# Optimization experiments

Measured on AMD Instinct MI355X. Metric: run time of the kernel, lower is better.

## Reference

```python
import jax, jax.numpy as jnp
import numpy as np

N_HEADS = 16  # emb_dim 512 // head_dim 32


def _heads(t, h=N_HEADS):
    b, n, d = t.shape
    return t.reshape(b, n, h, d // h).transpose(0, 2, 1, 3)  # [b h n hd]


def _merge(t):
    b, h, n, hd = t.shape
    return t.transpose(0, 2, 1, 3).reshape(b, n, h * hd)


def setup_inputs() -> dict:
    key = jax.random.key(0)
    ks = jax.random.split(key, 6)
    b, n, nc, d = 2, 2048, 256, 512
    x = jax.random.normal(ks[0], (b, n, d), dtype=jnp.float32)
    clusters = jax.random.normal(ks[1], (b, nc, d), dtype=jnp.float32)
    token_sizes = jax.random.uniform(ks[2], (b, n), dtype=jnp.float32)
    Wq = jax.random.normal(ks[3], (d, d), dtype=jnp.float32) * 0.02
    Wkv = jax.random.normal(ks[4], (d, 2 * d), dtype=jnp.float32) * 0.02
    Wo = jax.random.normal(ks[5], (d, d), dtype=jnp.float32) * 0.02
    return {"x": x, "clusters": clusters, "token_sizes": token_sizes,
            "Wq": Wq, "Wkv": Wkv, "Wo": Wo}


def reference(x, clusters, token_sizes, Wq, Wkv, Wo):
    b, n, d = x.shape
    hd = d // N_HEADS
    scale = hd ** -0.5

    q_in = jnp.concatenate([x, clusters], axis=1)       # pack tokens + clusters as queries
    q = _heads(q_in @ Wq)                               # [b h n+nc hd]
    kv = x @ Wkv                                        # [b n 2d]
    k = _heads(kv[..., :d])                             # [b h n hd]
    v = _heads(kv[..., d:])                             # [b h n hd]

    attn = jnp.einsum('bhqd,bhkd->bhqk', q, k) * scale  # [b h n+nc n]
    attn_x = attn[:, :, :n, :]                          # token queries  [b h n n]
    attn_c = attn[:, :, n:, :]                          # cluster queries [b h nc n]

    # soft assignment: softmax over cluster axis, then row-normalize
    a_c = jax.nn.softmax(attn_c, axis=-2)
    a_c = a_c / (jnp.sum(a_c, axis=-1, keepdims=True) + 1e-5)
    clusters_out = _merge(jnp.einsum('bhck,bhkd->bhcd', a_c, v)) @ Wo  # [b nc d]

    # additive log token-size bias on the query axis (as in the original)
    attn_x = attn_x + jnp.log(token_sizes + 1e-10)[:, None, :, None]
    a_x = jax.nn.softmax(attn_x, axis=-1)
    x_out = _merge(jnp.einsum('bhqk,bhkd->bhqd', a_x, v)) @ Wo  # [b n d]

    return x_out, clusters_out
```

## Files before the change

kernel.cpp:

```cpp
#include <hip/hip_runtime.h>
#include <hip/hip_bf16.h>

#define N_TOK 2048
#define N_CLU 256
#define N_ALL 2304
#define DMODEL 512
#define NH 16
#define HD 32
#define BATCH 2
#define EXPSCALE 0.25503486f

typedef short bf16x8 __attribute__((ext_vector_type(8)));
typedef float f32x4  __attribute__((ext_vector_type(4)));
typedef unsigned short u16;

static __device__ __forceinline__ u16 f2b(float x) {
    __hip_bfloat16 h = __float2bfloat16(x);
    return *reinterpret_cast<u16*>(&h);
}
static __device__ __forceinline__ unsigned int cvt_pk_bf16(float lo, float hi) {
    unsigned int r;
    asm("v_cvt_pk_bf16_f32 %0, %1, %2" : "=v"(r) : "v"(lo), "v"(hi));
    return r;
}
#if __has_builtin(__builtin_amdgcn_exp2f)
#define EXP2(x) __builtin_amdgcn_exp2f(x)
#else
#define EXP2(x) exp2f(x)
#endif
static __device__ __forceinline__ void async16(u16* lds, const u16* g) {
    __builtin_amdgcn_global_load_lds(
        (const __attribute__((address_space(1))) unsigned int*)g,
        (__attribute__((address_space(3))) unsigned int*)lds, 16, 0, 0);
}

__global__ __launch_bounds__(256) void cvt_bf16_k(const float* __restrict__ in,
                                                  u16* __restrict__ out)
{
    const long i = ((long)blockIdx.x * 256 + threadIdx.x) * 8;
    float4 a = *(const float4*)(in + i);
    float4 b = *(const float4*)(in + i + 4);
    u16 v[8] = { f2b(a.x), f2b(a.y), f2b(a.z), f2b(a.w),
                 f2b(b.x), f2b(b.y), f2b(b.z), f2b(b.w) };
    *(bf16x8*)(out + i) = *(const bf16x8*)v;
}

__global__ __launch_bounds__(256) void cvtT_k(const float* __restrict__ W,
                                              u16* __restrict__ WT,
                                              int R, int C, float scale)
{
    __shared__ float tile[32][33];
    const int tx = threadIdx.x & 31, ty = threadIdx.x >> 5;
    const int c0 = blockIdx.x * 32, r0 = blockIdx.y * 32;
    #pragma unroll
    for (int i = 0; i < 4; i++)
        tile[ty + i * 8][tx] = W[(long)(r0 + ty + i * 8) * C + c0 + tx];
    __syncthreads();
    #pragma unroll
    for (int i = 0; i < 4; i++)
        WT[(long)(c0 + ty + i * 8) * R + r0 + tx] = f2b(tile[tx][ty + i * 8] * scale);
}

__global__ __launch_bounds__(256) void gemm_bf16(
    const u16* __restrict__ A, long sA,
    const u16* __restrict__ BT,
    void* __restrict__ Cv, long sC,
    int N, int K, int mode)
{
    const int t = threadIdx.x;
    const int m0 = blockIdx.y * 128, n0 = blockIdx.x * 128;
    A += (long)blockIdx.z * sA;
    __shared__ u16 As[128 * 32];
    __shared__ u16 Bs[128 * 32];
    const int wid = t >> 6, lane = t & 63;
    const int lr = lane & 15, lg = lane >> 4;
    const int wr = wid >> 1, wc = wid & 1;
    f32x4 acc[4][4] = {};
    const int o1 = t * 16, o2 = o1 + 4096;
    const int row1 = o1 >> 6, ke1 = (o1 & 63) >> 1;
    const int row2 = o2 >> 6, ke2 = (o2 & 63) >> 1;
    for (int k0 = 0; k0 < K; k0 += 32) {
        async16(As + (o1 >> 1), A  + (long)(m0 + row1) * K + k0 + ke1);
        async16(As + (o2 >> 1), A  + (long)(m0 + row2) * K + k0 + ke2);
        async16(Bs + (o1 >> 1), BT + (long)(n0 + row1) * K + k0 + ke1);
        async16(Bs + (o2 >> 1), BT + (long)(n0 + row2) * K + k0 + ke2);
        __syncthreads();
        bf16x8 af[4], bfr[4];
        #pragma unroll
        for (int i = 0; i < 4; i++) {
            af[i]  = *(const bf16x8*)&As[(wr * 64 + i * 16 + lr) * 32 + lg * 8];
            bfr[i] = *(const bf16x8*)&Bs[(wc * 64 + i * 16 + lr) * 32 + lg * 8];
        }
        #pragma unroll
        for (int mi = 0; mi < 4; mi++)
            #pragma unroll
            for (int ni = 0; ni < 4; ni++)
                acc[mi][ni] = __builtin_amdgcn_mfma_f32_16x16x32_bf16(af[mi], bfr[ni], acc[mi][ni], 0, 0, 0);
        __syncthreads();
    }
    if (mode == 1) {
        float* C = (float*)Cv;
        #pragma unroll
        for (int mi = 0; mi < 4; mi++)
            #pragma unroll
            for (int ni = 0; ni < 4; ni++) {
                const int rbase = m0 + wr * 64 + mi * 16 + lg * 4;
                #pragma unroll
                for (int r = 0; r < 4; r++) {
                    int rw = rbase + r;
                    int bb = rw >= N_ALL;
                    int w  = rw - bb * N_ALL;
                    long orow = (w < N_TOK) ? ((long)bb * N_TOK + w)
                                            : (2L * N_TOK + (long)bb * N_CLU + (w - N_TOK));
                    C[orow * N + n0 + wc * 64 + ni * 16 + lr] = acc[mi][ni][r];
                }
            }
    } else {
        u16* C = (u16*)Cv + (long)blockIdx.z * sC;
        #pragma unroll
        for (int mi = 0; mi < 4; mi++)
            #pragma unroll
            for (int ni = 0; ni < 4; ni++) {
                const long rbase = m0 + wr * 64 + mi * 16 + lg * 4;
                #pragma unroll
                for (int r = 0; r < 4; r++)
                    C[(rbase + r) * N + n0 + wc * 64 + ni * 16 + lr] = f2b(acc[mi][ni][r]);
            }
    }
}

__global__ __launch_bounds__(256) void vt_prep(
    const u16* __restrict__ qkv, u16* __restrict__ vt)
{
    const int b = blockIdx.z, h = blockIdx.y, k0 = blockIdx.x * 64;
    const int t = threadIdx.x;
    __shared__ u16 tile[64][48];
    {
        const int key = t >> 2, dc = (t & 3) * 8;
        *(bf16x8*)&tile[key][dc] = *(const bf16x8*)(
            qkv + ((long)b * N_TOK + k0 + key) * 1536 + 1024 + h * HD + dc);
    }
    __syncthreads();
    {
        const int d = t & 31, kc = (t >> 5) * 8;
        bf16x8 v;
        #pragma unroll
        for (int i = 0; i < 8; i++) v[i] = (short)tile[kc + i][d];
        *(bf16x8*)(vt + (((long)(b * NH + h)) * HD + d) * N_TOK + k0 + kc) = v;
    }
}

__global__ __launch_bounds__(512) void attn_x3(
    const u16* __restrict__ qkv, const u16* __restrict__ vt,
    u16* __restrict__ aob)
{
    const int b = blockIdx.z, h = blockIdx.y;
    const int wid = threadIdx.x >> 6, lane = threadIdx.x & 63;
    const int lr = lane & 15, lg = lane >> 4;
    const int q0 = blockIdx.x * 128 + (wid & 3) * 32;
    const int khalf = wid >> 2;

    __shared__ unsigned int P[8][32][32];
    __shared__ float comb[4][64][18];
    __shared__ u16 Ot[4][32][40];

    unsigned int (*Pw)[32] = P[wid];
    const int sw = 4 * (lr & 7);

    bf16x8 qf[2];
    #pragma unroll
    for (int qs = 0; qs < 2; qs++)
        qf[qs] = *(const bf16x8*)(
            qkv + ((long)b * N_TOK + q0 + qs * 16 + lr) * 1536 + h * HD + lg * 8);

    f32x4 o[2][2] = {};
    float rs[2] = {0.f, 0.f};
    const u16* kbase = qkv + (long)b * N_TOK * 1536 + 512 + h * HD + lg * 8;
    const u16* vbase = vt + ((long)(b * NH + h)) * HD * N_TOK;

    const int kend = khalf * 1024 + 1024;
    for (int k0 = khalf * 1024; k0 < kend; k0 += 64) {
        bf16x8 kf[4];
        #pragma unroll
        for (int kg = 0; kg < 4; kg++)
            kf[kg] = *(const bf16x8*)(kbase + (long)(k0 + kg * 16 + lr) * 1536);
        #pragma unroll
        for (int qs = 0; qs < 2; qs++) {
            #pragma unroll
            for (int kg = 0; kg < 4; kg++) {
                f32x4 z = {0.f, 0.f, 0.f, 0.f};
                f32x4 s = __builtin_amdgcn_mfma_f32_16x16x32_bf16(kf[kg], qf[qs], z, 0, 0, 0);
                float e0 = EXP2(s[0]), e1 = EXP2(s[1]);
                float e2 = EXP2(s[2]), e3 = EXP2(s[3]);
                rs[qs] += (e0 + e1) + (e2 + e3);
                uint2 w = { cvt_pk_bf16(e0, e1), cvt_pk_bf16(e2, e3) };
                *(uint2*)&Pw[qs * 16 + lr][(kg * 8 + lg * 2) ^ sw] = w;
            }
        }
        #pragma unroll
        for (int c = 0; c < 2; c++) {
            bf16x8 pb0 = *(const bf16x8*)&Pw[lr][(c * 16 + lg * 4) ^ sw];
            bf16x8 pb1 = *(const bf16x8*)&Pw[16 + lr][(c * 16 + lg * 4) ^ sw];
            #pragma unroll
            for (int dg = 0; dg < 2; dg++) {
                bf16x8 vf = *(const bf16x8*)(
                    vbase + (long)(dg * 16 + lr) * N_TOK + k0 + c * 32 + lg * 8);
                o[0][dg] = __builtin_amdgcn_mfma_f32_16x16x32_bf16(vf, pb0, o[0][dg], 0, 0, 0);
                o[1][dg] = __builtin_amdgcn_mfma_f32_16x16x32_bf16(vf, pb1, o[1][dg], 0, 0, 0);
            }
        }
    }
    #pragma unroll
    for (int qs = 0; qs < 2; qs++) {
        rs[qs] += __shfl_xor(rs[qs], 16);
        rs[qs] += __shfl_xor(rs[qs], 32);
    }
    if (wid >= 4) {
        float* cp = &comb[wid - 4][lane][0];
        #pragma unroll
        for (int qs = 0; qs < 2; qs++)
            #pragma unroll
            for (int dg = 0; dg < 2; dg++)
                #pragma unroll
                for (int r = 0; r < 4; r++)
                    cp[qs * 8 + dg * 4 + r] = o[qs][dg][r];
        cp[16] = rs[0];
        cp[17] = rs[1];
    }
    __syncthreads();
    if (wid < 4) {
        const float* cp = &comb[wid][lane][0];
        #pragma unroll
        for (int qs = 0; qs < 2; qs++)
            #pragma unroll
            for (int dg = 0; dg < 2; dg++)
                #pragma unroll
                for (int r = 0; r < 4; r++)
                    o[qs][dg][r] += cp[qs * 8 + dg * 4 + r];
        rs[0] += cp[16];
        rs[1] += cp[17];
        const float inv0 = 1.f / rs[0], inv1 = 1.f / rs[1];
        #pragma unroll
        for (int dg = 0; dg < 2; dg++)
            #pragma unroll
            for (int r = 0; r < 4; r++) {
                Ot[wid][lr][dg * 16 + lg * 4 + r]      = f2b(o[0][dg][r] * inv0);
                Ot[wid][16 + lr][dg * 16 + lg * 4 + r] = f2b(o[1][dg][r] * inv1);
            }
        const int rrow = lane >> 2, seg = lane & 3;
        #pragma unroll
        for (int rep = 0; rep < 2; rep++) {
            bf16x8 v = *(const bf16x8*)&Ot[wid][rep * 16 + rrow][seg * 8];
            *(bf16x8*)(aob + ((long)b * N_ALL + q0 + rep * 16 + rrow) * DMODEL + h * HD + seg * 8) = v;
        }
    }
}

__global__ __launch_bounds__(256) void attn_c_mfma(
    const u16* __restrict__ qc, const u16* __restrict__ qkv,
    const u16* __restrict__ vt, float* __restrict__ part)
{
    const int b = blockIdx.z, h = blockIdx.y, kblk = blockIdx.x;
    const int wid = threadIdx.x >> 6, lane = threadIdx.x & 63;
    const int lr = lane & 15, lg = lane >> 4;
    const int c0 = wid * 64;

    __shared__ u16 Pl[4][64][72];
    __shared__ float cs2[64][4];
    u16 (*P)[72] = Pl[wid];

    bf16x8 qf[4];
    #pragma unroll
    for (int qs = 0; qs < 4; qs++)
        qf[qs] = *(const bf16x8*)(
            qc + ((long)(b * N_CLU) + c0 + qs * 16 + lr) * DMODEL + h * HD + lg * 8);

    f32x4 o[4][2] = {};
    float rs[4][4] = {};
    const u16* kbase = qkv + (long)b * N_TOK * 1536 + 512 + h * HD + lg * 8;
    const u16* vbase = vt + ((long)(b * NH + h)) * HD * N_TOK;

    for (int kt = 0; kt < 4; kt++) {
        const int k0 = kblk * 256 + kt * 64;
        bf16x8 kf[4];
        #pragma unroll
        for (int kg = 0; kg < 4; kg++)
            kf[kg] = *(const bf16x8*)(kbase + (long)(k0 + kg * 16 + lr) * 1536);
        f32x4 e[4][4];
        #pragma unroll
        for (int qs = 0; qs < 4; qs++)
            #pragma unroll
            for (int kg = 0; kg < 4; kg++) {
                f32x4 z = {0.f, 0.f, 0.f, 0.f};
                e[qs][kg] = __builtin_amdgcn_mfma_f32_16x16x32_bf16(qf[qs], kf[kg], z, 0, 0, 0);
            }
        float csum[4];
        #pragma unroll
        for (int kg = 0; kg < 4; kg++) {
            float v = 0.f;
            #pragma unroll
            for (int qs = 0; qs < 4; qs++)
                #pragma unroll
                for (int r = 0; r < 4; r++) {
                    float p = EXP2(e[qs][kg][r]);
                    e[qs][kg][r] = p;
                    v += p;
                }
            v += __shfl_xor(v, 16);
            v += __shfl_xor(v, 32);
            csum[kg] = v;
        }
        float own = (lg == 0) ? csum[0] : (lg == 1) ? csum[1] : (lg == 2) ? csum[2] : csum[3];
        __syncthreads();
        cs2[lane][wid] = own;
        __syncthreads();
        float ics0, ics1, ics2, ics3;
        {
            f32x4 c4;
            c4 = *(const f32x4*)&cs2[ 0 + lr][0]; ics0 = 1.f / (c4[0] + c4[1] + c4[2] + c4[3]);
            c4 = *(const f32x4*)&cs2[16 + lr][0]; ics1 = 1.f / (c4[0] + c4[1] + c4[2] + c4[3]);
            c4 = *(const f32x4*)&cs2[32 + lr][0]; ics2 = 1.f / (c4[0] + c4[1] + c4[2] + c4[3]);
            c4 = *(const f32x4*)&cs2[48 + lr][0]; ics3 = 1.f / (c4[0] + c4[1] + c4[2] + c4[3]);
        }
        #pragma unroll
        for (int qs = 0; qs < 4; qs++)
            #pragma unroll
            for (int kg = 0; kg < 4; kg++) {
                const float ics = (kg == 0) ? ics0 : (kg == 1) ? ics1 : (kg == 2) ? ics2 : ics3;
                #pragma unroll
                for (int r = 0; r < 4; r++) {
                    float p = e[qs][kg][r] * ics;
                    rs[qs][r] += p;
                    P[qs * 16 + lg * 4 + r][kg * 16 + lr] = f2b(p);
                }
            }
        #pragma unroll
        for (int kh = 0; kh < 2; kh++) {
            bf16x8 pf[4];
            #pragma unroll
            for (int qs = 0; qs < 4; qs++)
                pf[qs] = *(const bf16x8*)&P[qs * 16 + lr][kh * 32 + lg * 8];
            #pragma unroll
            for (int dg = 0; dg < 2; dg++) {
                bf16x8 vf = *(const bf16x8*)(
                    vbase + (long)(dg * 16 + lr) * N_TOK + k0 + kh * 32 + lg * 8);
                #pragma unroll
                for (int qs = 0; qs < 4; qs++)
                    o[qs][dg] = __builtin_amdgcn_mfma_f32_16x16x32_bf16(pf[qs], vf, o[qs][dg], 0, 0, 0);
            }
        }
    }
    float* pp = part + ((((long)(b * NH + h)) * 8 + kblk) * 256) * 36;
    #pragma unroll
    for (int qs = 0; qs < 4; qs++)
        #pragma unroll
        for (int r = 0; r < 4; r++) {
            const int row = c0 + qs * 16 + lg * 4 + r;
            pp[(long)row * 36 + lr]      = o[qs][0][r];
            pp[(long)row * 36 + 16 + lr] = o[qs][1][r];
            float v = rs[qs][r];
            v += __shfl_xor(v, 1); v += __shfl_xor(v, 2);
            v += __shfl_xor(v, 4); v += __shfl_xor(v, 8);
            if (lr == 0) pp[(long)row * 36 + 32] = v;
        }
}

__global__ __launch_bounds__(256) void attn_c_reduce(
    const float* __restrict__ part, u16* __restrict__ aob)
{
    const int gid = blockIdx.x * 256 + threadIdx.x;
    const int b = gid >> 12, h = (gid >> 8) & 15, c = gid & 255;
    float acc[32] = {};
    float rsum = 0.f;
    for (int j = 0; j < 8; j++) {
        const float* pp = part + ((((long)(b * NH + h)) * 8 + j) * 256 + c) * 36;
        #pragma unroll
        for (int e4 = 0; e4 < 8; e4++) {
            f32x4 v = *(const f32x4*)(pp + e4 * 4);
            acc[e4 * 4 + 0] += v[0]; acc[e4 * 4 + 1] += v[1];
            acc[e4 * 4 + 2] += v[2]; acc[e4 * 4 + 3] += v[3];
        }
        rsum += pp[32];
    }
    const float inv = 1.f / (rsum + 1e-5f);
    u16* orow = aob + ((long)b * N_ALL + N_TOK + c) * DMODEL + h * HD;
    #pragma unroll
    for (int e = 0; e < 32; e++) orow[e] = f2b(acc[e] * inv);
}

extern "C" void kernel_launch(void* const* d_in, const int* in_sizes, int n_in,
                              void* d_out, int out_size, void* d_ws, size_t ws_size,
                              hipStream_t stream)
{
    const float* x        = (const float*)d_in[0];
    const float* clusters = (const float*)d_in[1];
    const float* Wq  = (const float*)d_in[3];
    const float* Wkv = (const float*)d_in[4];
    const float* Wo  = (const float*)d_in[5];
    float* out = (float*)d_out;

    char* ws = (char*)d_ws;
    u16*   xb    = (u16*)(ws);
    u16*   cb    = (u16*)(ws + 4194304);
    u16*   WcatT = (u16*)(ws + 4718592);
    u16*   WoT   = (u16*)(ws + 6291456);
    u16*   qkv   = (u16*)(ws + 6815744);
    u16*   qc    = (u16*)(ws + 19398656);
    u16*   vt    = (u16*)(ws + 19922944);
    u16*   aob   = (u16*)(ws + 24117248);
    float* part  = (float*)(ws + 28835840);

    cvt_bf16_k<<<dim3(1024), 256, 0, stream>>>(x, xb);
    cvt_bf16_k<<<dim3(128),  256, 0, stream>>>(clusters, cb);
    cvtT_k<<<dim3(16, 16), 256, 0, stream>>>(Wq,  WcatT,             512,  512, EXPSCALE);
    cvtT_k<<<dim3(32, 16), 256, 0, stream>>>(Wkv, WcatT + 512 * 512, 512, 1024, 1.f);
    cvtT_k<<<dim3(16, 16), 256, 0, stream>>>(Wo,  WoT,               512,  512, 1.f);

    gemm_bf16<<<dim3(12, 16, 2), 256, 0, stream>>>(
        xb, (long)N_TOK * DMODEL, WcatT, qkv, (long)N_TOK * 1536, 1536, DMODEL, 0);
    gemm_bf16<<<dim3(4, 2, 2), 256, 0, stream>>>(
        cb, (long)N_CLU * DMODEL, WcatT, qc, (long)N_CLU * DMODEL, DMODEL, DMODEL, 0);

    vt_prep<<<dim3(32, 16, 2), 256, 0, stream>>>(qkv, vt);

    attn_x3<<<dim3(16, 16, 2), 512, 0, stream>>>(qkv, vt, aob);
    attn_c_mfma<<<dim3(8, 16, 2), 256, 0, stream>>>(qc, qkv, vt, part);
    attn_c_reduce<<<dim3(32), 256, 0, stream>>>(part, aob);

    gemm_bf16<<<dim3(4, 36, 1), 256, 0, stream>>>(
        aob, 0, WoT, out, 0, DMODEL, DMODEL, 1);
}
```

Baseline: 221.5 us.

## Split token attention key range four ways and widen cluster attention blocks

The token-query attention kernel now gives each block 64 queries and splits the key range across four waves per query group instead of two. That doubles the grid to raise occupancy and shorten each wave's serial loop. Partial outputs and row sums are combined through a shared-memory buffer that is reused from the P scratch space, which needs an extra barrier. The cluster attention kernel moves to 512 threads with 32 clusters per wave, which halves per-wave register state and widens the cross-wave column-sum reduction to eight entries.

```diff
diff --git a/kernel.cpp b/kernel.cpp
--- a/kernel.cpp
+++ b/kernel.cpp
@@ -150,51 +150,51 @@
     }
 }
 
-__global__ __launch_bounds__(512) void attn_x3(
+__global__ __launch_bounds__(512) void attn_x4(
     const u16* __restrict__ qkv, const u16* __restrict__ vt,
     u16* __restrict__ aob)
 {
     const int b = blockIdx.z, h = blockIdx.y;
     const int wid = threadIdx.x >> 6, lane = threadIdx.x & 63;
     const int lr = lane & 15, lg = lane >> 4;
-    const int q0 = blockIdx.x * 128 + (wid & 3) * 32;
-    const int khalf = wid >> 2;
-
-    __shared__ unsigned int P[8][32][32];
-    __shared__ float comb[4][64][18];
-    __shared__ u16 Ot[4][32][40];
-
-    unsigned int (*Pw)[32] = P[wid];
+    const int qs = wid & 1, kq = wid >> 1;
+    const int q0 = blockIdx.x * 64 + qs * 32;
+
+    __shared__ __align__(16) char smem[32768];
+    unsigned int (*Pw)[32] = (unsigned int (*)[32])(smem + wid * 4096);
+    float* combB = (float*)smem;
+    u16*   OtB   = (u16*)(smem + 27648);
+
     const int sw = 4 * (lr & 7);
 
     bf16x8 qf[2];
     #pragma unroll
-    for (int qs = 0; qs < 2; qs++)
-        qf[qs] = *(const bf16x8*)(
-            qkv + ((long)b * N_TOK + q0 + qs * 16 + lr) * 1536 + h * HD + lg * 8);
+    for (int qq = 0; qq < 2; qq++)
+        qf[qq] = *(const bf16x8*)(
+            qkv + ((long)b * N_TOK + q0 + qq * 16 + lr) * 1536 + h * HD + lg * 8);
 
     f32x4 o[2][2] = {};
     float rs[2] = {0.f, 0.f};
     const u16* kbase = qkv + (long)b * N_TOK * 1536 + 512 + h * HD + lg * 8;
     const u16* vbase = vt + ((long)(b * NH + h)) * HD * N_TOK;
 
-    const int kend = khalf * 1024 + 1024;
-    for (int k0 = khalf * 1024; k0 < kend; k0 += 64) {
+    const int kstart = kq * 512;
+    for (int k0 = kstart; k0 < kstart + 512; k0 += 64) {
         bf16x8 kf[4];
         #pragma unroll
         for (int kg = 0; kg < 4; kg++)
             kf[kg] = *(const bf16x8*)(kbase + (long)(k0 + kg * 16 + lr) * 1536);
         #pragma unroll
-        for (int qs = 0; qs < 2; qs++) {
+        for (int qq = 0; qq < 2; qq++) {
             #pragma unroll
             for (int kg = 0; kg < 4; kg++) {
                 f32x4 z = {0.f, 0.f, 0.f, 0.f};
-                f32x4 s = __builtin_amdgcn_mfma_f32_16x16x32_bf16(kf[kg], qf[qs], z, 0, 0, 0);
+                f32x4 s = __builtin_amdgcn_mfma_f32_16x16x32_bf16(kf[kg], qf[qq], z, 0, 0, 0);
                 float e0 = EXP2(s[0]), e1 = EXP2(s[1]);
                 float e2 = EXP2(s[2]), e3 = EXP2(s[3]);
-                rs[qs] += (e0 + e1) + (e2 + e3);
+                rs[qq] += (e0 + e1) + (e2 + e3);
                 uint2 w = { cvt_pk_bf16(e0, e1), cvt_pk_bf16(e2, e3) };
-                *(uint2*)&Pw[qs * 16 + lr][(kg * 8 + lg * 2) ^ sw] = w;
+                *(uint2*)&Pw[qq * 16 + lr][(kg * 8 + lg * 2) ^ sw] = w;
             }
         }
         #pragma unroll
@@ -211,72 +211,77 @@
         }
     }
     #pragma unroll
-    for (int qs = 0; qs < 2; qs++) {
-        rs[qs] += __shfl_xor(rs[qs], 16);
-        rs[qs] += __shfl_xor(rs[qs], 32);
-    }
-    if (wid >= 4) {
-        float* cp = &comb[wid - 4][lane][0];
-        #pragma unroll
-        for (int qs = 0; qs < 2; qs++)
+    for (int qq = 0; qq < 2; qq++) {
+        rs[qq] += __shfl_xor(rs[qq], 16);
+        rs[qq] += __shfl_xor(rs[qq], 32);
+    }
+    __syncthreads();
+    if (kq > 0) {
+        float* cp = combB + (((qs * 3 + kq - 1) * 64) + lane) * 18;
+        #pragma unroll
+        for (int qq = 0; qq < 2; qq++)
             #pragma unroll
             for (int dg = 0; dg < 2; dg++)
                 #pragma unroll
                 for (int r = 0; r < 4; r++)
-                    cp[qs * 8 + dg * 4 + r] = o[qs][dg][r];
+                    cp[qq * 8 + dg * 4 + r] = o[qq][dg][r];
         cp[16] = rs[0];
         cp[17] = rs[1];
     }
     __syncthreads();
-    if (wid < 4) {
-        const float* cp = &comb[wid][lane][0];
-        #pragma unroll
-        for (int qs = 0; qs < 2; qs++)
-            #pragma unroll
-            for (int dg = 0; dg < 2; dg++)
-                #pragma unroll
-                for (int r = 0; r < 4; r++)
-                    o[qs][dg][r] += cp[qs * 8 + dg * 4 + r];
-        rs[0] += cp[16];
-        rs[1] += cp[17];
+    if (kq == 0) {
+        #pragma unroll
+        for (int j = 0; j < 3; j++) {
+            const float* cp = combB + (((qs * 3 + j) * 64) + lane) * 18;
+            #pragma unroll
+            for (int qq = 0; qq < 2; qq++)
+                #pragma unroll
+                for (int dg = 0; dg < 2; dg++)
+                    #pragma unroll
+                    for (int r = 0; r < 4; r++)
+                        o[qq][dg][r] += cp[qq * 8 + dg * 4 + r];
+            rs[0] += cp[16];
+            rs[1] += cp[17];
+        }
         const float inv0 = 1.f / rs[0], inv1 = 1.f / rs[1];
+        u16* Ot = OtB + qs * 32 * 40;
         #pragma unroll
         for (int dg = 0; dg < 2; dg++)
             #pragma unroll
             for (int r = 0; r < 4; r++) {
-                Ot[wid][lr][dg * 16 + lg * 4 + r]      = f2b(o[0][dg][r] * inv0);
-                Ot[wid][16 + lr][dg * 16 + lg * 4 + r] = f2b(o[1][dg][r] * inv1);
+                Ot[lr * 40 + dg * 16 + lg * 4 + r]        = f2b(o[0][dg][r] * inv0);
+                Ot[(16 + lr) * 40 + dg * 16 + lg * 4 + r] = f2b(o[1][dg][r] * inv1);
             }
         const int rrow = lane >> 2, seg = lane & 3;
         #pragma unroll
         for (int rep = 0; rep < 2; rep++) {
-            bf16x8 v = *(const bf16x8*)&Ot[wid][rep * 16 + rrow][seg * 8];
+            bf16x8 v = *(const bf16x8*)&Ot[(rep * 16 + rrow) * 40 + seg * 8];
             *(bf16x8*)(aob + ((long)b * N_ALL + q0 + rep * 16 + rrow) * DMODEL + h * HD + seg * 8) = v;
         }
     }
 }
 
-__global__ __launch_bounds__(256) void attn_c_mfma(
+__global__ __launch_bounds__(512) void attn_c_mfma(
     const u16* __restrict__ qc, const u16* __restrict__ qkv,
     const u16* __restrict__ vt, float* __restrict__ part)
 {
     const int b = blockIdx.z, h = blockIdx.y, kblk = blockIdx.x;
     const int wid = threadIdx.x >> 6, lane = threadIdx.x & 63;
     const int lr = lane & 15, lg = lane >> 4;
-    const int c0 = wid * 64;
-
-    __shared__ u16 Pl[4][64][72];
-    __shared__ float cs2[64][4];
+    const int c0 = wid * 32;
+
+    __shared__ u16 Pl[8][32][72];
+    __shared__ float cs2[64][8];
     u16 (*P)[72] = Pl[wid];
 
-    bf16x8 qf[4];
-    #pragma unroll
-    for (int qs = 0; qs < 4; qs++)
+    bf16x8 qf[2];
+    #pragma unroll
+    for (int qs = 0; qs < 2; qs++)
         qf[qs] = *(const bf16x8*)(
             qc + ((long)(b * N_CLU) + c0 + qs * 16 + lr) * DMODEL + h * HD + lg * 8);
 
-    f32x4 o[4][2] = {};
-    float rs[4][4] = {};
+    f32x4 o[2][2] = {};
+    float rs[2][4] = {};
     const u16* kbase = qkv + (long)b * N_TOK * 1536 + 512 + h * HD + lg * 8;
     const u16* vbase = vt + ((long)(b * NH + h)) * HD * N_TOK;
 
@@ -286,9 +291,9 @@
         #pragma unroll
         for (int kg = 0; kg < 4; kg++)
             kf[kg] = *(const bf16x8*)(kbase + (long)(k0 + kg * 16 + lr) * 1536);
-        f32x4 e[4][4];
-        #pragma unroll
-        for (int qs = 0; qs < 4; qs++)
+        f32x4 e[2][4];
+        #pragma unroll
+        for (int qs = 0; qs < 2; qs++)
             #pragma unroll
             for (int kg = 0; kg < 4; kg++) {
                 f32x4 z = {0.f, 0.f, 0.f, 0.f};
@@ -299,7 +304,7 @@
         for (int kg = 0; kg < 4; kg++) {
             float v = 0.f;
             #pragma unroll
-            for (int qs = 0; qs < 4; qs++)
+            for (int qs = 0; qs < 2; qs++)
                 #pragma unroll
                 for (int r = 0; r < 4; r++) {
                     float p = EXP2(e[qs][kg][r]);
@@ -314,45 +319,43 @@
         __syncthreads();
         cs2[lane][wid] = own;
         __syncthreads();
-        float ics0, ics1, ics2, ics3;
-        {
-            f32x4 c4;
-            c4 = *(const f32x4*)&cs2[ 0 + lr][0]; ics0 = 1.f / (c4[0] + c4[1] + c4[2] + c4[3]);
-            c4 = *(const f32x4*)&cs2[16 + lr][0]; ics1 = 1.f / (c4[0] + c4[1] + c4[2] + c4[3]);
-            c4 = *(const f32x4*)&cs2[32 + lr][0]; ics2 = 1.f / (c4[0] + c4[1] + c4[2] + c4[3]);
-            c4 = *(const f32x4*)&cs2[48 + lr][0]; ics3 = 1.f / (c4[0] + c4[1] + c4[2] + c4[3]);
-        }
-        #pragma unroll
-        for (int qs = 0; qs < 4; qs++)
+        float ics[4];
+        #pragma unroll
+        for (int kg = 0; kg < 4; kg++) {
+            f32x4 a = *(const f32x4*)&cs2[kg * 16 + lr][0];
+            f32x4 c = *(const f32x4*)&cs2[kg * 16 + lr][4];
+            ics[kg] = 1.f / ((a[0] + a[1] + a[2] + a[3]) + (c[0] + c[1] + c[2] + c[3]));
+        }
+        #pragma unroll
+        for (int qs = 0; qs < 2; qs++)
             #pragma unroll
             for (int kg = 0; kg < 4; kg++) {
-                const float ics = (kg == 0) ? ics0 : (kg == 1) ? ics1 : (kg == 2) ? ics2 : ics3;
                 #pragma unroll
                 for (int r = 0; r < 4; r++) {
-                    float p = e[qs][kg][r] * ics;
+                    float p = e[qs][kg][r] * ics[kg];
                     rs[qs][r] += p;
                     P[qs * 16 + lg * 4 + r][kg * 16 + lr] = f2b(p);
                 }
             }
         #pragma unroll
         for (int kh = 0; kh < 2; kh++) {
-            bf16x8 pf[4];
-            #pragma unroll
-            for (int qs = 0; qs < 4; qs++)
+            bf16x8 pf[2];
+            #pragma unroll
+            for (int qs = 0; qs < 2; qs++)
                 pf[qs] = *(const bf16x8*)&P[qs * 16 + lr][kh * 32 + lg * 8];
             #pragma unroll
             for (int dg = 0; dg < 2; dg++) {
                 bf16x8 vf = *(const bf16x8*)(
                     vbase + (long)(dg * 16 + lr) * N_TOK + k0 + kh * 32 + lg * 8);
                 #pragma unroll
-                for (int qs = 0; qs < 4; qs++)
+                for (int qs = 0; qs < 2; qs++)
                     o[qs][dg] = __builtin_amdgcn_mfma_f32_16x16x32_bf16(pf[qs], vf, o[qs][dg], 0, 0, 0);
             }
         }
     }
     float* pp = part + ((((long)(b * NH + h)) * 8 + kblk) * 256) * 36;
     #pragma unroll
-    for (int qs = 0; qs < 4; qs++)
+    for (int qs = 0; qs < 2; qs++)
         #pragma unroll
         for (int r = 0; r < 4; r++) {
             const int row = c0 + qs * 16 + lg * 4 + r;
@@ -423,8 +426,8 @@
 
     vt_prep<<<dim3(32, 16, 2), 256, 0, stream>>>(qkv, vt);
 
-    attn_x3<<<dim3(16, 16, 2), 512, 0, stream>>>(qkv, vt, aob);
-    attn_c_mfma<<<dim3(8, 16, 2), 256, 0, stream>>>(qc, qkv, vt, part);
+    attn_x4<<<dim3(32, 16, 2), 512, 0, stream>>>(qkv, vt, aob);
+    attn_c_mfma<<<dim3(8, 16, 2), 512, 0, stream>>>(qc, qkv, vt, part);
     attn_c_reduce<<<dim3(32), 256, 0, stream>>>(part, aob);
 
     gemm_bf16<<<dim3(4, 36, 1), 256, 0, stream>>>(
```

Result: no change. 221.0 us (-0.2%).
